# Optimization experiments

Measured on AMD Instinct MI355X. Metric: run time of the kernel, lower is better.

Reference implementation:

```python
import jax, jax.numpy as jnp
import numpy as np

D_MODEL = 1024
NUM_HEADS = 16
D_K = D_MODEL // NUM_HEADS
B, S = 4, 2048
NEG = -1e9


def setup_inputs() -> dict:
    key = jax.random.key(0)
    ks = jax.random.split(key, 12)
    def lin(kw, kb):
        bound = 1.0 / np.sqrt(D_MODEL)
        W = jax.random.uniform(kw, (D_MODEL, D_MODEL), jnp.float32, -bound, bound)
        b = jax.random.uniform(kb, (D_MODEL,), jnp.float32, -bound, bound)
        return W, b
    Wq, bq = lin(ks[0], ks[1])
    Wk, bk = lin(ks[2], ks[3])
    Wv, bv = lin(ks[4], ks[5])
    Wo, bo = lin(ks[6], ks[7])
    Q = jax.random.normal(ks[8], (B, S, D_MODEL), jnp.float32)
    K = jax.random.normal(ks[9], (B, S, D_MODEL), jnp.float32)
    V = jax.random.normal(ks[10], (B, S, D_MODEL), jnp.float32)
    # causal mask: 1 = keep, 0 = masked
    mask = jnp.tril(jnp.ones((S, S), jnp.int32))[None, None, :, :]
    mask = jnp.broadcast_to(mask, (B, 1, S, S))
    return {"Q": Q, "K": K, "V": V, "mask": mask,
            "Wq": Wq, "bq": bq, "Wk": Wk, "bk": bk,
            "Wv": Wv, "bv": bv, "Wo": Wo, "bo": bo}


def _split_heads(x):
    b, s, _ = x.shape
    return x.reshape(b, s, NUM_HEADS, D_K).transpose(0, 2, 1, 3)  # [B,H,S,Dk]


def reference(Q, K, V, mask, Wq, bq, Wk, bk, Wv, bv, Wo, bo):
    q = _split_heads(Q @ Wq.T + bq)
    k = _split_heads(K @ Wk.T + bk)
    v = _split_heads(V @ Wv.T + bv)
    scores = jnp.einsum('bhqd,bhkd->bhqk', q, k) / jnp.sqrt(jnp.float32(D_K))
    scores = jnp.where(mask == 0, jnp.float32(NEG), scores)
    probs = jax.nn.softmax(scores, axis=-1)
    attn = jnp.einsum('bhqk,bhkd->bhqd', probs, v)  # [B,H,S,Dk]
    attn = attn.transpose(0, 2, 1, 3).reshape(Q.shape[0], Q.shape[1], D_MODEL)
    return attn @ Wo.T + bo
```

## Files before the change

### kernel.cpp

```cpp
#include <hip/hip_runtime.h>
#include <hip/hip_bf16.h>
#include <cstdint>

typedef float floatx4 __attribute__((ext_vector_type(4)));
typedef __bf16 bf16x8 __attribute__((ext_vector_type(8)));
typedef unsigned short ushort8 __attribute__((ext_vector_type(8)));

#define AS_G __attribute__((address_space(1)))
#define AS_L __attribute__((address_space(3)))

__device__ __forceinline__ void async_cp16(const void* g, void* l) {
    __builtin_amdgcn_global_load_lds((const AS_G uint32_t*)g, (AS_L uint32_t*)l, 16, 0, 0);
}

__device__ __forceinline__ floatx4 mfma16x16x32(bf16x8 a, bf16x8 b, floatx4 c) {
    return __builtin_amdgcn_mfma_f32_16x16x32_bf16(a, b, c, 0, 0, 0);
}

__device__ __forceinline__ unsigned short f2bf(float x) {
    return __builtin_bit_cast(unsigned short, (__bf16)x);
}

__global__ __launch_bounds__(256) void cvt4_f32_bf16(const float* __restrict__ a, const float* __restrict__ b,
                                                     const float* __restrict__ c, const float* __restrict__ d,
                                                     unsigned short* __restrict__ out, int n) {
    const float* in = blockIdx.y == 0 ? a : blockIdx.y == 1 ? b : blockIdx.y == 2 ? c : d;
    unsigned short* o = out + (size_t)blockIdx.y * n;
    int i = (blockIdx.x * 256 + threadIdx.x) * 4;
    if (i >= n) return;
    float4 v = *(const float4*)(in + i);
    ushort4 u;
    u.x = f2bf(v.x); u.y = f2bf(v.y); u.z = f2bf(v.z); u.w = f2bf(v.w);
    *(ushort4*)(o + i) = u;
}

template <int MODE>
__global__ __launch_bounds__(256) void gemm_f32a(const float* __restrict__ A,
                                                 const unsigned short* __restrict__ W,
                                                 const float* __restrict__ bias,
                                                 float oscale,
                                                 unsigned short* __restrict__ outp) {
    __shared__ unsigned short As[64 * 64];
    __shared__ unsigned short Bs[128 * 64];
    const int tid  = threadIdx.x;
    const int wave = tid >> 6, lane = tid & 63;
    const int quad = lane >> 4, l15 = lane & 15;
    const int l7   = l15 & 7;
    const int m0 = blockIdx.x * 64, n0 = blockIdx.y * 128;
    const int waveM = (wave >> 1) * 32, waveN = (wave & 1) * 64;
    const int r8  = lane >> 3;
    const int gsw = (lane & 7) ^ r8;

    floatx4 acc[2][4] = {};
    float4 pre[2][2];

#pragma unroll
    for (int c4 = 0; c4 < 2; ++c4) {
        const int row = (wave + c4 * 4) * 8 + r8;
        const float* src = A + (size_t)(m0 + row) * 1024 + gsw * 8;
        pre[c4][0] = *(const float4*)src;
        pre[c4][1] = *(const float4*)(src + 4);
    }

    for (int k0 = 0; k0 < 1024; k0 += 64) {
#pragma unroll
        for (int c4 = 0; c4 < 2; ++c4) {
            const int c = wave + c4 * 4;
            ushort8 v;
            v[0] = f2bf(pre[c4][0].x); v[1] = f2bf(pre[c4][0].y);
            v[2] = f2bf(pre[c4][0].z); v[3] = f2bf(pre[c4][0].w);
            v[4] = f2bf(pre[c4][1].x); v[5] = f2bf(pre[c4][1].y);
            v[6] = f2bf(pre[c4][1].z); v[7] = f2bf(pre[c4][1].w);
            *(ushort8*)((char*)As + c * 1024 + lane * 16) = v;
        }
#pragma unroll
        for (int c4 = 0; c4 < 4; ++c4) {
            const int c = wave + c4 * 4;
            const int row = c * 8 + r8;
            async_cp16(W + (size_t)(n0 + row) * 1024 + k0 + gsw * 8, (char*)Bs + c * 1024);
        }
        if (k0 < 960) {
#pragma unroll
            for (int c4 = 0; c4 < 2; ++c4) {
                const int row = (wave + c4 * 4) * 8 + r8;
                const float* src = A + (size_t)(m0 + row) * 1024 + (k0 + 64) + gsw * 8;
                pre[c4][0] = *(const float4*)src;
                pre[c4][1] = *(const float4*)(src + 4);
            }
            asm volatile("s_waitcnt vmcnt(4) lgkmcnt(0)" ::: "memory");
        } else {
            asm volatile("s_waitcnt vmcnt(0) lgkmcnt(0)" ::: "memory");
        }
        __builtin_amdgcn_s_barrier();
        __builtin_amdgcn_sched_barrier(0);

#pragma unroll
        for (int h = 0; h < 2; ++h) {
            const int g = (quad + h * 4) ^ l7;
            bf16x8 af[2], bf[4];
#pragma unroll
            for (int t = 0; t < 2; ++t)
                af[t] = *(const bf16x8*)&As[(waveM + t * 16 + l15) * 64 + g * 8];
#pragma unroll
            for (int t = 0; t < 4; ++t)
                bf[t] = *(const bf16x8*)&Bs[(waveN + t * 16 + l15) * 64 + g * 8];
#pragma unroll
            for (int mt = 0; mt < 2; ++mt)
#pragma unroll
                for (int nt = 0; nt < 4; ++nt)
                    acc[mt][nt] = mfma16x16x32(af[mt], bf[nt], acc[mt][nt]);
        }

        asm volatile("s_waitcnt lgkmcnt(0)" ::: "memory");
        __builtin_amdgcn_sched_barrier(0);
        __builtin_amdgcn_s_barrier();
    }

#pragma unroll
    for (int mt = 0; mt < 2; ++mt) {
#pragma unroll
        for (int nt = 0; nt < 4; ++nt) {
            const int gcol = n0 + waveN + nt * 16 + l15;
            const float bv = bias[gcol];
#pragma unroll
            for (int r = 0; r < 4; ++r) {
                const int grow = m0 + waveM + mt * 16 + quad * 4 + r;
                const float val = (acc[mt][nt][r] + bv) * oscale;
                const int b = grow >> 11, s = grow & 2047;
                const int h = gcol >> 6, dk = gcol & 63;
                const size_t idx = (MODE == 1) ? ((size_t)(b * 16 + h) * 64 + dk) * 2048 + s
                                               : ((size_t)(b * 16 + h) * 2048 + s) * 64 + dk;
                outp[idx] = f2bf(val);
            }
        }
    }
}

__global__ __launch_bounds__(256) void gemm_out(const unsigned short* __restrict__ A,
                                                const unsigned short* __restrict__ W,
                                                const float* __restrict__ bias,
                                                float* __restrict__ outv) {
    __shared__ unsigned short As[64 * 64];
    __shared__ unsigned short Bs[128 * 64];
    const int tid  = threadIdx.x;
    const int wave = tid >> 6, lane = tid & 63;
    const int quad = lane >> 4, l15 = lane & 15;
    const int l7   = l15 & 7;
    const int m0 = blockIdx.x * 64, n0 = blockIdx.y * 128;
    const int waveM = (wave >> 1) * 32, waveN = (wave & 1) * 64;
    const int r8  = lane >> 3;
    const int gsw = (lane & 7) ^ r8;

    floatx4 acc[2][4] = {};

    for (int k0 = 0; k0 < 1024; k0 += 64) {
        for (int c = wave; c < 8; c += 4)
            async_cp16(A + (size_t)(m0 + c * 8 + r8) * 1024 + k0 + gsw * 8, (char*)As + c * 1024);
        for (int c = wave; c < 16; c += 4)
            async_cp16(W + (size_t)(n0 + c * 8 + r8) * 1024 + k0 + gsw * 8, (char*)Bs + c * 1024);
        __syncthreads();

#pragma unroll
        for (int h = 0; h < 2; ++h) {
            const int g = (quad + h * 4) ^ l7;
            bf16x8 af[2], bf[4];
#pragma unroll
            for (int t = 0; t < 2; ++t)
                af[t] = *(const bf16x8*)&As[(waveM + t * 16 + l15) * 64 + g * 8];
#pragma unroll
            for (int t = 0; t < 4; ++t)
                bf[t] = *(const bf16x8*)&Bs[(waveN + t * 16 + l15) * 64 + g * 8];
#pragma unroll
            for (int mt = 0; mt < 2; ++mt)
#pragma unroll
                for (int nt = 0; nt < 4; ++nt)
                    acc[mt][nt] = mfma16x16x32(af[mt], bf[nt], acc[mt][nt]);
        }
        __syncthreads();
    }

#pragma unroll
    for (int mt = 0; mt < 2; ++mt) {
#pragma unroll
        for (int nt = 0; nt < 4; ++nt) {
            const int gcol = n0 + waveN + nt * 16 + l15;
            const float bv = bias[gcol];
#pragma unroll
            for (int r = 0; r < 4; ++r) {
                const int grow = m0 + waveM + mt * 16 + quad * 4 + r;
                outv[(size_t)grow * 1024 + gcol] = acc[mt][nt][r] + bv;
            }
        }
    }
}

#define PS_STRIDE 72

template <bool DOA, bool DIAGA, bool DIAGB>
__device__ __forceinline__ void pair_tiles(const bf16x8 kf[4][2], const bf16x8 vf[2][4],
                                           unsigned short* __restrict__ PswB,
                                           unsigned short* __restrict__ PswA,
                                           bf16x8 qfB0, bf16x8 qfB1,
                                           bf16x8 qfA0, bf16x8 qfA1,
                                           int quad, int l15,
                                           int qrowB, int qrowA, int kv0,
                                           float* __restrict__ lsumB, float* __restrict__ lsumA,
                                           floatx4* __restrict__ OB, floatx4* __restrict__ OA) {
    floatx4 scB[4], scA[4];
    __builtin_amdgcn_s_setprio(1);
#pragma unroll
    for (int kvt = 0; kvt < 4; ++kvt) {
        floatx4 b = {};
        b = mfma16x16x32(qfB0, kf[kvt][0], b);
        scB[kvt] = b;
        if (DOA) {
            floatx4 a = {};
            a = mfma16x16x32(qfA0, kf[kvt][0], a);
            scA[kvt] = a;
        }
    }
#pragma unroll
    for (int kvt = 0; kvt < 4; ++kvt) {
        scB[kvt] = mfma16x16x32(qfB1, kf[kvt][1], scB[kvt]);
        if (DOA) scA[kvt] = mfma16x16x32(qfA1, kf[kvt][1], scA[kvt]);
    }
    __builtin_amdgcn_s_setprio(0);

#pragma unroll
    for (int kvt = 0; kvt < 4; ++kvt) {
#pragma unroll
        for (int r = 0; r < 4; ++r) {
            float s = scB[kvt][r];
            if (DIAGB && (kv0 + kvt * 16 + l15 > qrowB + r)) s = -1.0e9f;
            const float p = __builtin_amdgcn_exp2f(s);
            lsumB[r] += p;
            PswB[(quad * 4 + r) * PS_STRIDE + kvt * 16 + l15] = f2bf(p);
        }
    }
    __builtin_amdgcn_s_setprio(1);
#pragma unroll
    for (int half = 0; half < 2; ++half) {
        bf16x8 pf = *(const bf16x8*)&PswB[l15 * PS_STRIDE + half * 32 + quad * 8];
#pragma unroll
        for (int nt = 0; nt < 4; ++nt)
            OB[nt] = mfma16x16x32(pf, vf[half][nt], OB[nt]);
    }
    __builtin_amdgcn_s_setprio(0);

    if (DOA) {
#pragma unroll
        for (int kvt = 0; kvt < 4; ++kvt) {
#pragma unroll
            for (int r = 0; r < 4; ++r) {
                float s = scA[kvt][r];
                if (DIAGA && (kv0 + kvt * 16 + l15 > qrowA + r)) s = -1.0e9f;
                const float p = __builtin_amdgcn_exp2f(s);
                lsumA[r] += p;
                PswA[(quad * 4 + r) * PS_STRIDE + kvt * 16 + l15] = f2bf(p);
            }
        }
        __builtin_amdgcn_s_setprio(1);
#pragma unroll
        for (int half = 0; half < 2; ++half) {
            bf16x8 pf = *(const bf16x8*)&PswA[l15 * PS_STRIDE + half * 32 + quad * 8];
#pragma unroll
            for (int nt = 0; nt < 4; ++nt)
                OA[nt] = mfma16x16x32(pf, vf[half][nt], OA[nt]);
        }
        __builtin_amdgcn_s_setprio(0);
    }
}

__global__ __launch_bounds__(256, 2) void flash_causal(const unsigned short* __restrict__ qp,
                                                       const unsigned short* __restrict__ kp,
                                                       const unsigned short* __restrict__ vt,
                                                       unsigned short* __restrict__ attn) {
    __shared__ unsigned short Ks[2][64 * 64];
    __shared__ unsigned short Vs[2][64 * 64];
    __shared__ unsigned short PsB[4 * 16 * PS_STRIDE];
    __shared__ unsigned short PsA[4 * 16 * PS_STRIDE];

    const int tid  = threadIdx.x;
    const int wave = tid >> 6, lane = tid & 63;
    const int quad = lane >> 4, l15 = lane & 15;
    const int l7   = l15 & 7;
    const int bh = blockIdx.x;
    const int pr = blockIdx.y;
    const int tA = pr, tB = 31 - pr;

    unsigned short* PswB = &PsB[wave * 16 * PS_STRIDE];
    unsigned short* PswA = &PsA[wave * 16 * PS_STRIDE];

    bf16x8 qfA0, qfA1, qfB0, qfB1;
    {
        const unsigned short* qa = qp + ((size_t)bh * 2048 + tA * 64 + wave * 16 + l15) * 64;
        qfA0 = *(const bf16x8*)(qa + quad * 8);
        qfA1 = *(const bf16x8*)(qa + 32 + quad * 8);
        const unsigned short* qb = qp + ((size_t)bh * 2048 + tB * 64 + wave * 16 + l15) * 64;
        qfB0 = *(const bf16x8*)(qb + quad * 8);
        qfB1 = *(const bf16x8*)(qb + 32 + quad * 8);
    }

    float lsumA[4] = {}, lsumB[4] = {};
    floatx4 OA[4] = {}, OB[4] = {};

    const int qrowA = tA * 64 + wave * 16 + quad * 4;
    const int qrowB = tB * 64 + wave * 16 + quad * 4;

    const int r8  = lane >> 3;
    const int gsw = (lane & 7) ^ r8;
    const size_t kb = (size_t)bh * 131072;
    const size_t vb = (size_t)bh * 64 * 2048;

#define STAGE(t, b) do {                                                                  \
        const int kv0_ = (t) * 64;                                                        \
        for (int c = wave; c < 8; c += 4) {                                               \
            const int row_ = c * 8 + r8;                                                  \
            async_cp16(kp + kb + (size_t)(kv0_ + row_) * 64 + gsw * 8,                    \
                       (char*)Ks[b] + c * 1024);                                          \
            async_cp16(vt + vb + (size_t)row_ * 2048 + kv0_ + gsw * 8,                    \
                       (char*)Vs[b] + c * 1024);                                          \
        } } while (0)

    STAGE(0, 0);

    int buf = 0;
    for (int t = 0; t <= tB; ++t) {
        if (t < tB) {
            STAGE(t + 1, buf ^ 1);
            asm volatile("s_waitcnt vmcnt(4)" ::: "memory");
        } else {
            asm volatile("s_waitcnt vmcnt(0)" ::: "memory");
        }
        __builtin_amdgcn_s_barrier();
        __builtin_amdgcn_sched_barrier(0);

        const unsigned short* Kc = Ks[buf];
        const unsigned short* Vc = Vs[buf];

        bf16x8 kf[4][2], vf[2][4];
        const int g1 = quad ^ l7, g2 = (quad + 4) ^ l7;
#pragma unroll
        for (int kvt = 0; kvt < 4; ++kvt) {
            kf[kvt][0] = *(const bf16x8*)&Kc[(kvt * 16 + l15) * 64 + g1 * 8];
            kf[kvt][1] = *(const bf16x8*)&Kc[(kvt * 16 + l15) * 64 + g2 * 8];
        }
#pragma unroll
        for (int half = 0; half < 2; ++half) {
            const int gb = (quad + half * 4) ^ l7;
#pragma unroll
            for (int nt = 0; nt < 4; ++nt)
                vf[half][nt] = *(const bf16x8*)&Vc[(nt * 16 + l15) * 64 + gb * 8];
        }

        const int kv0 = t * 64;
        if (t < tA)
            pair_tiles<true , false, false>(kf, vf, PswB, PswA, qfB0, qfB1, qfA0, qfA1,
                                            quad, l15, qrowB, qrowA, kv0, lsumB, lsumA, OB, OA);
        else if (t == tA)
            pair_tiles<true , true , false>(kf, vf, PswB, PswA, qfB0, qfB1, qfA0, qfA1,
                                            quad, l15, qrowB, qrowA, kv0, lsumB, lsumA, OB, OA);
        else if (t < tB)
            pair_tiles<false, false, false>(kf, vf, PswB, PswA, qfB0, qfB1, qfA0, qfA1,
                                            quad, l15, qrowB, qrowA, kv0, lsumB, lsumA, OB, OA);
        else
            pair_tiles<false, false, true >(kf, vf, PswB, PswA, qfB0, qfB1, qfA0, qfA1,
                                            quad, l15, qrowB, qrowA, kv0, lsumB, lsumA, OB, OA);

        asm volatile("s_waitcnt lgkmcnt(0)" ::: "memory");
        __builtin_amdgcn_sched_barrier(0);
        __builtin_amdgcn_s_barrier();
        buf ^= 1;
    }
#undef STAGE

    const int b = bh >> 4, h = bh & 15;
#pragma unroll
    for (int r = 0; r < 4; ++r) {
        float lA = lsumA[r], lB = lsumB[r];
#pragma unroll
        for (int off = 8; off; off >>= 1) {
            lA += __shfl_xor(lA, off, 16);
            lB += __shfl_xor(lB, off, 16);
        }
        const float invA = 1.0f / lA;
        const float invB = 1.0f / lB;
        const size_t rbA = ((size_t)b * 2048 + qrowA + r) * 1024 + h * 64;
        const size_t rbB = ((size_t)b * 2048 + qrowB + r) * 1024 + h * 64;
#pragma unroll
        for (int nt = 0; nt < 4; ++nt) {
            attn[rbA + nt * 16 + l15] = f2bf(OA[nt][r] * invA);
            attn[rbB + nt * 16 + l15] = f2bf(OB[nt][r] * invB);
        }
    }
}

extern "C" void kernel_launch(void* const* d_in, const int* in_sizes, int n_in,
                              void* d_out, int out_size, void* d_ws, size_t ws_size,
                              hipStream_t stream) {
    const float* Q  = (const float*)d_in[0];
    const float* K  = (const float*)d_in[1];
    const float* V  = (const float*)d_in[2];
    const float* Wq = (const float*)d_in[4];  const float* bq = (const float*)d_in[5];
    const float* Wk = (const float*)d_in[6];  const float* bk = (const float*)d_in[7];
    const float* Wv = (const float*)d_in[8];  const float* bv = (const float*)d_in[9];
    const float* Wo = (const float*)d_in[10]; const float* bo = (const float*)d_in[11];
    float* out = (float*)d_out;

    const int NIN = 8192 * 1024;
    const int NW  = 1024 * 1024;

    unsigned short* ws   = (unsigned short*)d_ws;
    unsigned short* wb   = ws;
    unsigned short* qp   = wb + 4 * NW;
    unsigned short* kp   = qp + NIN;
    unsigned short* vtp  = kp + NIN;
    unsigned short* attnb = vtp + NIN;

    const float QSCL = 0.125f * 1.44269504088896f;

    dim3 blk(256);
    dim3 gcvtW((NW + 1023) / 1024, 4);
    dim3 ggemm(128, 8);
    dim3 gflash(64, 16);

    cvt4_f32_bf16<<<gcvtW, blk, 0, stream>>>(Wq, Wk, Wv, Wo, wb, NW);

    gemm_f32a<0><<<ggemm, blk, 0, stream>>>(Q, wb + 0 * NW, bq, QSCL, qp);
    gemm_f32a<0><<<ggemm, blk, 0, stream>>>(K, wb + 1 * NW, bk, 1.0f, kp);
    gemm_f32a<1><<<ggemm, blk, 0, stream>>>(V, wb + 2 * NW, bv, 1.0f, vtp);

    flash_causal<<<gflash, blk, 0, stream>>>(qp, kp, vtp, attnb);

    gemm_out<<<ggemm, blk, 0, stream>>>(attnb, wb + 3 * NW, bo, out);
}
```

Before: 353.8 us.

## Load GEMM operand fragments directly from global memory, dropping LDS staging

Both projection GEMM kernels stop staging A and W tiles through shared memory. Each wave now loads its MFMA fragments straight from global memory, converting fp32 activations to bf16 in registers, and the barriers are removed. This cuts LDS traffic and synchronisation, but gives up the cross-wave sharing of tiles and the software prefetch. Global and L2 traffic rises, and each load is a 16-byte per-lane strided access whose latency is no longer hidden.

Result: slower. 663.6 us (+87.5%).

```diff
diff --git a/kernel.cpp b/kernel.cpp
--- a/kernel.cpp
+++ b/kernel.cpp
@@ -40,80 +40,41 @@
                                                  const float* __restrict__ bias,
                                                  float oscale,
                                                  unsigned short* __restrict__ outp) {
-    __shared__ unsigned short As[64 * 64];
-    __shared__ unsigned short Bs[128 * 64];
     const int tid  = threadIdx.x;
     const int wave = tid >> 6, lane = tid & 63;
     const int quad = lane >> 4, l15 = lane & 15;
-    const int l7   = l15 & 7;
     const int m0 = blockIdx.x * 64, n0 = blockIdx.y * 128;
     const int waveM = (wave >> 1) * 32, waveN = (wave & 1) * 64;
-    const int r8  = lane >> 3;
-    const int gsw = (lane & 7) ^ r8;
 
     floatx4 acc[2][4] = {};
-    float4 pre[2][2];
-
-#pragma unroll
-    for (int c4 = 0; c4 < 2; ++c4) {
-        const int row = (wave + c4 * 4) * 8 + r8;
-        const float* src = A + (size_t)(m0 + row) * 1024 + gsw * 8;
-        pre[c4][0] = *(const float4*)src;
-        pre[c4][1] = *(const float4*)(src + 4);
-    }
+
+    const float* Ab = A + (size_t)(m0 + waveM + l15) * 1024 + quad * 8;
+    const unsigned short* Wb = W + (size_t)(n0 + waveN + l15) * 1024 + quad * 8;
 
     for (int k0 = 0; k0 < 1024; k0 += 64) {
 #pragma unroll
-        for (int c4 = 0; c4 < 2; ++c4) {
-            const int c = wave + c4 * 4;
-            ushort8 v;
-            v[0] = f2bf(pre[c4][0].x); v[1] = f2bf(pre[c4][0].y);
-            v[2] = f2bf(pre[c4][0].z); v[3] = f2bf(pre[c4][0].w);
-            v[4] = f2bf(pre[c4][1].x); v[5] = f2bf(pre[c4][1].y);
-            v[6] = f2bf(pre[c4][1].z); v[7] = f2bf(pre[c4][1].w);
-            *(ushort8*)((char*)As + c * 1024 + lane * 16) = v;
-        }
-#pragma unroll
-        for (int c4 = 0; c4 < 4; ++c4) {
-            const int c = wave + c4 * 4;
-            const int row = c * 8 + r8;
-            async_cp16(W + (size_t)(n0 + row) * 1024 + k0 + gsw * 8, (char*)Bs + c * 1024);
-        }
-        if (k0 < 960) {
-#pragma unroll
-            for (int c4 = 0; c4 < 2; ++c4) {
-                const int row = (wave + c4 * 4) * 8 + r8;
-                const float* src = A + (size_t)(m0 + row) * 1024 + (k0 + 64) + gsw * 8;
-                pre[c4][0] = *(const float4*)src;
-                pre[c4][1] = *(const float4*)(src + 4);
+        for (int h = 0; h < 2; ++h) {
+            const int kk = k0 + h * 32;
+            bf16x8 af[2], bf[4];
+#pragma unroll
+            for (int t = 0; t < 2; ++t) {
+                const float* src = Ab + (size_t)t * 16 * 1024 + kk;
+                float4 lo = *(const float4*)src;
+                float4 hi = *(const float4*)(src + 4);
+                bf16x8 v;
+                v[0] = (__bf16)lo.x; v[1] = (__bf16)lo.y; v[2] = (__bf16)lo.z; v[3] = (__bf16)lo.w;
+                v[4] = (__bf16)hi.x; v[5] = (__bf16)hi.y; v[6] = (__bf16)hi.z; v[7] = (__bf16)hi.w;
+                af[t] = v;
             }
-            asm volatile("s_waitcnt vmcnt(4) lgkmcnt(0)" ::: "memory");
-        } else {
-            asm volatile("s_waitcnt vmcnt(0) lgkmcnt(0)" ::: "memory");
-        }
-        __builtin_amdgcn_s_barrier();
-        __builtin_amdgcn_sched_barrier(0);
-
-#pragma unroll
-        for (int h = 0; h < 2; ++h) {
-            const int g = (quad + h * 4) ^ l7;
-            bf16x8 af[2], bf[4];
-#pragma unroll
-            for (int t = 0; t < 2; ++t)
-                af[t] = *(const bf16x8*)&As[(waveM + t * 16 + l15) * 64 + g * 8];
 #pragma unroll
             for (int t = 0; t < 4; ++t)
-                bf[t] = *(const bf16x8*)&Bs[(waveN + t * 16 + l15) * 64 + g * 8];
+                bf[t] = *(const bf16x8*)(Wb + (size_t)t * 16 * 1024 + kk);
 #pragma unroll
             for (int mt = 0; mt < 2; ++mt)
 #pragma unroll
                 for (int nt = 0; nt < 4; ++nt)
                     acc[mt][nt] = mfma16x16x32(af[mt], bf[nt], acc[mt][nt]);
         }
-
-        asm volatile("s_waitcnt lgkmcnt(0)" ::: "memory");
-        __builtin_amdgcn_sched_barrier(0);
-        __builtin_amdgcn_s_barrier();
     }
 
 #pragma unroll
@@ -140,43 +101,34 @@
                                                 const unsigned short* __restrict__ W,
                                                 const float* __restrict__ bias,
                                                 float* __restrict__ outv) {
-    __shared__ unsigned short As[64 * 64];
-    __shared__ unsigned short Bs[128 * 64];
     const int tid  = threadIdx.x;
     const int wave = tid >> 6, lane = tid & 63;
     const int quad = lane >> 4, l15 = lane & 15;
-    const int l7   = l15 & 7;
     const int m0 = blockIdx.x * 64, n0 = blockIdx.y * 128;
     const int waveM = (wave >> 1) * 32, waveN = (wave & 1) * 64;
-    const int r8  = lane >> 3;
-    const int gsw = (lane & 7) ^ r8;
 
     floatx4 acc[2][4] = {};
 
+    const unsigned short* Ab = A + (size_t)(m0 + waveM + l15) * 1024 + quad * 8;
+    const unsigned short* Wb = W + (size_t)(n0 + waveN + l15) * 1024 + quad * 8;
+
     for (int k0 = 0; k0 < 1024; k0 += 64) {
-        for (int c = wave; c < 8; c += 4)
-            async_cp16(A + (size_t)(m0 + c * 8 + r8) * 1024 + k0 + gsw * 8, (char*)As + c * 1024);
-        for (int c = wave; c < 16; c += 4)
-            async_cp16(W + (size_t)(n0 + c * 8 + r8) * 1024 + k0 + gsw * 8, (char*)Bs + c * 1024);
-        __syncthreads();
-
 #pragma unroll
         for (int h = 0; h < 2; ++h) {
-            const int g = (quad + h * 4) ^ l7;
+            const int kk = k0 + h * 32;
             bf16x8 af[2], bf[4];
 #pragma unroll
             for (int t = 0; t < 2; ++t)
-                af[t] = *(const bf16x8*)&As[(waveM + t * 16 + l15) * 64 + g * 8];
+                af[t] = *(const bf16x8*)(Ab + (size_t)t * 16 * 1024 + kk);
 #pragma unroll
             for (int t = 0; t < 4; ++t)
-                bf[t] = *(const bf16x8*)&Bs[(waveN + t * 16 + l15) * 64 + g * 8];
+                bf[t] = *(const bf16x8*)(Wb + (size_t)t * 16 * 1024 + kk);
 #pragma unroll
             for (int mt = 0; mt < 2; ++mt)
 #pragma unroll
                 for (int nt = 0; nt < 4; ++nt)
                     acc[mt][nt] = mfma16x16x32(af[mt], bf[nt], acc[mt][nt]);
         }
-        __syncthreads();
     }
 
 #pragma unroll
```
